# Kernel tuning notes

Measured on AMD Instinct MI355X. Metric: run time of the kernel, lower is better.

Reference implementation:

```python
import jax, jax.numpy as jnp
import numpy as np

B, L, T = 64, 128, 48
E, HE, H = 512, 1024, 1024


def setup_inputs() -> dict:
    key = jax.random.key(0)
    ks = jax.random.split(key, 20)
    s = 0.02
    inp = {
        'enc_hiddens': jax.random.normal(ks[0], (B, L, HE), jnp.float32),
        'enc_masks': jax.random.randint(ks[1], (B, L), 0, 2, jnp.int32),
        'h1_init': jax.random.normal(ks[2], (B, H), jnp.float32),
        'c1_init': jax.random.normal(ks[3], (B, H), jnp.float32),
        'h2_init': jax.random.normal(ks[4], (B, H), jnp.float32),
        'c2_init': jax.random.normal(ks[5], (B, H), jnp.float32),
        'captions': jax.random.normal(ks[6], (T, B, E), jnp.float32),
        # LSTMCell 1: input E -> hidden H
        'W_ih1': jax.random.normal(ks[7], (4 * H, E), jnp.float32) * s,
        'W_hh1': jax.random.normal(ks[8], (4 * H, H), jnp.float32) * s,
        'b_ih1': jnp.zeros((4 * H,), jnp.float32),
        'b_hh1': jnp.zeros((4 * H,), jnp.float32),
        # LSTMCell 2: input 2H -> hidden H
        'W_ih2': jax.random.normal(ks[9], (4 * H, 2 * H), jnp.float32) * s,
        'W_hh2': jax.random.normal(ks[10], (4 * H, H), jnp.float32) * s,
        'b_ih2': jnp.zeros((4 * H,), jnp.float32),
        'b_hh2': jnp.zeros((4 * H,), jnp.float32),
        # att_projection: He -> H
        'W_att': jax.random.normal(ks[11], (H, HE), jnp.float32) * s,
        'b_att': jnp.zeros((H,), jnp.float32),
        # combined_output_projection: He+H -> H
        'W_comb': jax.random.normal(ks[12], (H, HE + H), jnp.float32) * s,
        'b_comb': jnp.zeros((H,), jnp.float32),
    }
    return inp


def _lstm_cell(x, h, c, W_ih, W_hh, b_ih, b_hh):
    gates = x @ W_ih.T + b_ih + h @ W_hh.T + b_hh  # (B, 4H)
    i, f, g, o = jnp.split(gates, 4, axis=-1)
    i = jax.nn.sigmoid(i)
    f = jax.nn.sigmoid(f)
    g = jnp.tanh(g)
    o = jax.nn.sigmoid(o)
    c_new = f * c + i * g
    h_new = o * jnp.tanh(c_new)
    return h_new, c_new


def reference(enc_hiddens, enc_masks, h1_init, c1_init, h2_init, c2_init, captions,
              W_ih1, W_hh1, b_ih1, b_hh1, W_ih2, W_hh2, b_ih2, b_hh2,
              W_att, b_att, W_comb, b_comb):
    # Precompute attention projection of encoder hiddens: (B, L, H)
    enc_proj = jnp.einsum('blf,hf->blh', enc_hiddens, W_att) + b_att
    mask = enc_masks.astype(bool)  # True -> masked with -inf
    o0 = jnp.zeros((enc_hiddens.shape[0], W_hh1.shape[1]), enc_hiddens.dtype)

    def step(carry, elem):
        h1, c1, h2, c2, o_prev = carry
        h1, c1 = _lstm_cell(elem, h1, c1, W_ih1, W_hh1, b_ih1, b_hh1)
        bar = jnp.concatenate([h1, o_prev], axis=1)  # (B, 2H)
        h2, c2 = _lstm_cell(bar, h2, c2, W_ih2, W_hh2, b_ih2, b_hh2)
        e_t = jnp.einsum('bh,blh->bl', h2, enc_proj)
        e_t = jnp.where(mask, -jnp.inf, e_t)
        alpha = jax.nn.softmax(e_t, axis=1)
        a_t = jnp.einsum('bl,blf->bf', alpha, enc_hiddens)  # (B, He)
        U_t = jnp.concatenate([a_t, h2], axis=1)
        o_t = jnp.tanh(U_t @ W_comb.T + b_comb)  # dropout is identity in eval
        return (h1, c1, h2, c2, o_t), o_t

    _, outs = jax.lax.scan(step, (h1_init, c1_init, h2_init, c2_init, o0), captions)
    return outs  # (T, B, H)
```

## Files before the change

kernel.cpp:

```cpp
#include <hip/hip_runtime.h>

static constexpr int Bn = 64, Ln = 128, Tn = 48, En = 512, HEn = 1024, Hn = 1024, Gn = 4096;

typedef _Float16 h16;
typedef __attribute__((ext_vector_type(8))) _Float16 h16x8;
typedef __attribute__((ext_vector_type(2))) _Float16 h16x2;
typedef __attribute__((ext_vector_type(4))) float f32x4;

__device__ __forceinline__ float sigf(float x){ return 1.f / (1.f + expf(-x)); }

__device__ __forceinline__ h16x8 ldnt(const h16* p){
#if __has_builtin(__builtin_nontemporal_load)
  return __builtin_nontemporal_load(reinterpret_cast<const h16x8*>(p));
#else
  return *reinterpret_cast<const h16x8*>(p);
#endif
}

struct CvtJobs {
  const float* src[8];
  h16x2* dst[8];
  int n2[8];
};

__global__ void cvt_all(CvtJobs jobs){
  int stride = gridDim.x * blockDim.x;
  int gid = blockIdx.x * blockDim.x + threadIdx.x;
  #pragma unroll
  for (int s = 0; s < 8; s++){
    const float* src = jobs.src[s];
    h16x2* dst = jobs.dst[s];
    int n2 = jobs.n2[s];
    for (int i = gid; i < n2; i += stride){
      float2 v = reinterpret_cast<const float2*>(src)[i];
      h16x2 o; o.x = (h16)v.x; o.y = (h16)v.y;
      dst[i] = o;
    }
  }
}

__global__ void init_state(const float* __restrict__ h1i, const float* __restrict__ c1i,
                           const float* __restrict__ h2i, const float* __restrict__ c2i,
                           h16* __restrict__ h1a, float* __restrict__ c1,
                           h16* __restrict__ h2a, float* __restrict__ c2,
                           float* __restrict__ h2f, h16* __restrict__ oh){
  int i = blockIdx.x * blockDim.x + threadIdx.x;
  if (i < Bn * Hn){
    h1a[i] = (h16)h1i[i]; c1[i] = c1i[i];
    h2a[i] = (h16)h2i[i]; c2[i] = c2i[i];
    h2f[i] = h2i[i];
    oh[i] = (h16)0.f;
  }
}

__global__ __launch_bounds__(256, 2) void gemm_lds(
    const h16* __restrict__ A, int lda,
    const h16* __restrict__ Bw, int ldb,
    const float* __restrict__ bias0, const float* __restrict__ bias1,
    float* __restrict__ outF, h16* __restrict__ outH, int ldc, int K)
{
  __shared__ __align__(16) h16 sA[2][4096];
  __shared__ __align__(16) h16 sB[2][4096];
  int tid = threadIdx.x;
  int w = tid >> 6, lane = tid & 63;
  int la = lane & 15, q = lane >> 4;
  int wr = w >> 1, wc = w & 1;
  int m0 = blockIdx.x * 128, n0 = blockIdx.y * 128;

  int srow = tid >> 2, sq = tid & 3;
  const h16* gAa = A + (size_t)(m0 + srow) * lda + sq * 8;
  const h16* gAb = gAa + (size_t)64 * lda;
  const h16* gBa = Bw + (size_t)(n0 + srow) * ldb + sq * 8;
  const h16* gBb = gBa + (size_t)64 * ldb;
  int dO = sq * 1024 + srow * 8;

  f32x4 acc[4][4];
  #pragma unroll
  for (int i = 0; i < 4; i++)
    #pragma unroll
    for (int j = 0; j < 4; j++) acc[i][j] = (f32x4){0.f, 0.f, 0.f, 0.f};

  h16x8 rAa, rAb, rBa, rBb;
  auto GLOAD = [&](int kt){
    int k0 = kt * 32;
    rAa = *reinterpret_cast<const h16x8*>(gAa + k0);
    rAb = *reinterpret_cast<const h16x8*>(gAb + k0);
    rBa = *reinterpret_cast<const h16x8*>(gBa + k0);
    rBb = *reinterpret_cast<const h16x8*>(gBb + k0);
  };
  auto SWRITE = [&](int buf){
    *reinterpret_cast<h16x8*>(&sA[buf][dO])       = rAa;
    *reinterpret_cast<h16x8*>(&sA[buf][dO + 512]) = rAb;
    *reinterpret_cast<h16x8*>(&sB[buf][dO])       = rBa;
    *reinterpret_cast<h16x8*>(&sB[buf][dO + 512]) = rBb;
  };

  int NT = K / 32;
  GLOAD(0); SWRITE(0);
  GLOAD(1);
  __syncthreads();
  for (int t = 0; t < NT; t++){
    int buf = t & 1;
    h16x8 af[4], bf[4];
    #pragma unroll
    for (int mi = 0; mi < 4; mi++)
      af[mi] = *reinterpret_cast<const h16x8*>(&sA[buf][q * 1024 + (wr * 64 + mi * 16 + la) * 8]);
    #pragma unroll
    for (int ni = 0; ni < 4; ni++)
      bf[ni] = *reinterpret_cast<const h16x8*>(&sB[buf][q * 1024 + (wc * 64 + ni * 16 + la) * 8]);
    #pragma unroll
    for (int mi = 0; mi < 4; mi++)
      #pragma unroll
      for (int ni = 0; ni < 4; ni++)
        acc[mi][ni] = __builtin_amdgcn_mfma_f32_16x16x32_f16(af[mi], bf[ni], acc[mi][ni], 0, 0, 0);
    if (t + 1 < NT){
      __syncthreads();
      SWRITE((t + 1) & 1);
      if (t + 2 < NT) GLOAD(t + 2);
      __syncthreads();
    }
  }

  #pragma unroll
  for (int mi = 0; mi < 4; mi++){
    int mrow = m0 + wr * 64 + mi * 16 + q * 4;
    #pragma unroll
    for (int ni = 0; ni < 4; ni++){
      int n = n0 + wc * 64 + ni * 16 + la;
      float bs = (bias0 ? bias0[n] : 0.f) + (bias1 ? bias1[n] : 0.f);
      #pragma unroll
      for (int r = 0; r < 4; r++){
        float v = acc[mi][ni][r] + bs;
        size_t off = (size_t)(mrow + r) * ldc + n;
        if (outF) outF[off] = v;
        else      outH[off] = (h16)v;
      }
    }
  }
}

struct PBuf { h16x8 a0, a1, a2, a3, b; };

__device__ __forceinline__ void pld(PBuf& p, const h16* __restrict__ Ap,
                                    const h16* __restrict__ Bp, int k){
  p.a0 = *reinterpret_cast<const h16x8*>(Ap + k);
  p.a1 = *reinterpret_cast<const h16x8*>(Ap + 16 * Hn + k);
  p.a2 = *reinterpret_cast<const h16x8*>(Ap + 32 * Hn + k);
  p.a3 = *reinterpret_cast<const h16x8*>(Ap + 48 * Hn + k);
  p.b  = *reinterpret_cast<const h16x8*>(Bp + k);
}
__device__ __forceinline__ void pmm(const PBuf& p, f32x4* acc){
  acc[0] = __builtin_amdgcn_mfma_f32_16x16x32_f16(p.a0, p.b, acc[0], 0, 0, 0);
  acc[1] = __builtin_amdgcn_mfma_f32_16x16x32_f16(p.a1, p.b, acc[1], 0, 0, 0);
  acc[2] = __builtin_amdgcn_mfma_f32_16x16x32_f16(p.a2, p.b, acc[2], 0, 0, 0);
  acc[3] = __builtin_amdgcn_mfma_f32_16x16x32_f16(p.a3, p.b, acc[3], 0, 0, 0);
}

template<int NS>
__device__ __forceinline__ void gseg_pf(const h16* __restrict__ Ap,
                                        const h16* __restrict__ Bp, f32x4* acc){
  PBuf p0, p1, p2, p3;
  pld(p0, Ap, Bp, 0);
  pld(p1, Ap, Bp, 32);
  pld(p2, Ap, Bp, 64);
  pld(p3, Ap, Bp, 96);
  #pragma unroll 1
  for (int s = 0; s + 4 < NS; s += 4){
    pmm(p0, acc); pld(p0, Ap, Bp, (s + 4) * 32);
    pmm(p1, acc); pld(p1, Ap, Bp, (s + 5) * 32);
    pmm(p2, acc); pld(p2, Ap, Bp, (s + 6) * 32);
    pmm(p3, acc); pld(p3, Ap, Bp, (s + 7) * 32);
  }
  pmm(p0, acc); pmm(p1, acc); pmm(p2, acc); pmm(p3, acc);
}

struct PBuf2 { h16x8 a0, a1, b; };

__device__ __forceinline__ void pld2(PBuf2& p, const h16* __restrict__ Ap,
                                     const h16* __restrict__ Bp, int k){
  p.a0 = *reinterpret_cast<const h16x8*>(Ap + k);
  p.a1 = *reinterpret_cast<const h16x8*>(Ap + 16 * Hn + k);
  p.b  = ldnt(Bp + k);
}
__device__ __forceinline__ void pmm2(const PBuf2& p, f32x4* acc){
  acc[0] = __builtin_amdgcn_mfma_f32_16x16x32_f16(p.a0, p.b, acc[0], 0, 0, 0);
  acc[1] = __builtin_amdgcn_mfma_f32_16x16x32_f16(p.a1, p.b, acc[1], 0, 0, 0);
}

template<int NS>
__device__ __forceinline__ void gseg2_pf(const h16* __restrict__ Ap,
                                         const h16* __restrict__ Bp, f32x4* acc){
  PBuf2 p0, p1, p2, p3;
  pld2(p0, Ap, Bp, 0);
  pld2(p1, Ap, Bp, 32);
  pld2(p2, Ap, Bp, 64);
  pld2(p3, Ap, Bp, 96);
  #pragma unroll 1
  for (int s = 0; s + 4 < NS; s += 4){
    pmm2(p0, acc); pld2(p0, Ap, Bp, (s + 4) * 32);
    pmm2(p1, acc); pld2(p1, Ap, Bp, (s + 5) * 32);
    pmm2(p2, acc); pld2(p2, Ap, Bp, (s + 6) * 32);
    pmm2(p3, acc); pld2(p3, Ap, Bp, (s + 7) * 32);
  }
  pmm2(p0, acc); pmm2(p1, acc); pmm2(p2, acc); pmm2(p3, acc);
}

__global__ __launch_bounds__(512, 1) void kA(
    const h16* __restrict__ h1cur, const h16* __restrict__ h2prev, const h16* __restrict__ oh,
    h16* __restrict__ h1next, h16* __restrict__ h2cur, float* __restrict__ h2f,
    float* __restrict__ c1, float* __restrict__ c2,
    const h16* __restrict__ wih2, const h16* __restrict__ whh2, const h16* __restrict__ whh1,
    const float* __restrict__ bih2, const float* __restrict__ bhh2,
    const float* __restrict__ pre1_t, int mode)
{
  __shared__ float sg[4][2][32][17];
  int bid = blockIdx.x, tid = threadIdx.x;
  int wv = tid >> 6, lane = tid & 63;
  int g = wv & 3, kh = wv >> 2;
  int la = lane & 15, q = lane >> 4;
  bool is2 = (mode == 1) && (bid < 128);
  int unit = is2 ? bid : (mode == 1 ? bid - 128 : bid);
  int jb = unit & 63, mh = unit >> 6;
  int j0 = jb * 16;
  int r0 = mh * 32;
  bool active = is2 || (pre1_t != nullptr);

  if (active){
    f32x4 acc[2];
    acc[0] = (f32x4){0.f, 0.f, 0.f, 0.f};
    acc[1] = (f32x4){0.f, 0.f, 0.f, 0.f};
    int n0 = g * 1024 + j0;
    size_t aoff = (size_t)(r0 + la) * Hn + q * 8;
    if (is2){
      if (kh == 0){
        gseg2_pf<32>(h1cur + aoff, wih2 + (size_t)(n0 + la) * 2048 + q * 8,        acc);
        gseg2_pf<16>(oh    + aoff, wih2 + (size_t)(n0 + la) * 2048 + 1024 + q * 8, acc);
      } else {
        gseg2_pf<16>(oh     + aoff + 512, wih2 + (size_t)(n0 + la) * 2048 + 1536 + q * 8, acc);
        gseg2_pf<32>(h2prev + aoff,       whh2 + (size_t)(n0 + la) * 1024 + q * 8,        acc);
      }
    } else {
      if (kh == 0)
        gseg2_pf<16>(h1cur + aoff,       whh1 + (size_t)(n0 + la) * 1024 + q * 8,       acc);
      else
        gseg2_pf<16>(h1cur + aoff + 512, whh1 + (size_t)(n0 + la) * 1024 + 512 + q * 8, acc);
    }
    #pragma unroll
    for (int mi = 0; mi < 2; mi++)
      #pragma unroll
      for (int r = 0; r < 4; r++)
        sg[g][kh][mi * 16 + q * 4 + r][la] = acc[mi][r];
  }
  __syncthreads();
  if (active && tid < 512){
    int e = tid;
    int rl = e >> 4, col = e & 15, j = j0 + col;
    int row = r0 + rl;
    float gi = sg[0][0][rl][col] + sg[0][1][rl][col];
    float gf = sg[1][0][rl][col] + sg[1][1][rl][col];
    float gg = sg[2][0][rl][col] + sg[2][1][rl][col];
    float go = sg[3][0][rl][col] + sg[3][1][rl][col];
    if (is2){
      gi += bih2[j] + bhh2[j];
      gf += bih2[j + 1024] + bhh2[j + 1024];
      gg += bih2[j + 2048] + bhh2[j + 2048];
      go += bih2[j + 3072] + bhh2[j + 3072];
      float c_ = sigf(gf) * c2[row * Hn + j] + sigf(gi) * tanhf(gg);
      c2[row * Hn + j] = c_;
      float h_ = sigf(go) * tanhf(c_);
      h2cur[row * Hn + j] = (h16)h_;
      h2f[row * Hn + j] = h_;
    } else {
      const float* p = pre1_t + (size_t)row * Gn;
      gi += p[j]; gf += p[j + 1024]; gg += p[j + 2048]; go += p[j + 3072];
      float c_ = sigf(gf) * c1[row * Hn + j] + sigf(gi) * tanhf(gg);
      c1[row * Hn + j] = c_;
      h1next[row * Hn + j] = (h16)(sigf(go) * tanhf(c_));
    }
  }
}

__global__ __launch_bounds__(256, 2) void kB(
    const float* __restrict__ h2f, const h16* __restrict__ eph, const int* __restrict__ msk,
    float* __restrict__ ebuf,
    const h16* __restrict__ h2cur, const h16* __restrict__ wcomb, const float* __restrict__ bcomb,
    float* __restrict__ hwb)
{
  int bid = blockIdx.x, tid = threadIdx.x;
  int w = tid >> 6, lane = tid & 63;
  if (bid >= 16){
    int n = bid - 16;
    int b = n & 63;
    int l = (n >> 6) * 4 + w;
    const f32x4* h2r = reinterpret_cast<const f32x4*>(h2f + (size_t)b * Hn + lane * 16);
    f32x4 hv0 = h2r[0], hv1 = h2r[1], hv2 = h2r[2], hv3 = h2r[3];
    const h16x8* er = reinterpret_cast<const h16x8*>(eph + ((size_t)b * Ln + l) * Hn + lane * 16);
    h16x8 e0 = er[0], e1 = er[1];
    float acc = 0.f;
    #pragma unroll
    for (int i = 0; i < 4; i++) acc += hv0[i] * (float)e0[i];
    #pragma unroll
    for (int i = 0; i < 4; i++) acc += hv1[i] * (float)e0[4 + i];
    #pragma unroll
    for (int i = 0; i < 4; i++) acc += hv2[i] * (float)e1[i];
    #pragma unroll
    for (int i = 0; i < 4; i++) acc += hv3[i] * (float)e1[4 + i];
    for (int off = 32; off; off >>= 1) acc += __shfl_xor(acc, off);
    if (lane == 0) ebuf[b * Ln + l] = msk[b * Ln + l] ? -1e30f : acc;
  } else {
    int hb = bid;
    int la = lane & 15, q = lane >> 4;
    int n0 = hb * 64 + w * 16;
    f32x4 acc[4];
    #pragma unroll
    for (int mi = 0; mi < 4; mi++) acc[mi] = (f32x4){0.f, 0.f, 0.f, 0.f};
    gseg_pf<32>(h2cur + la * Hn + q * 8,
                wcomb + (size_t)(n0 + la) * (HEn + Hn) + HEn + q * 8, acc);
    float bs = bcomb[n0 + la];
    #pragma unroll
    for (int mi = 0; mi < 4; mi++)
      #pragma unroll
      for (int r = 0; r < 4; r++)
        hwb[(size_t)(mi * 16 + q * 4 + r) * Hn + n0 + la] = acc[mi][r] + bs;
  }
}

__global__ __launch_bounds__(256, 2) void kC(
    int t, const float* __restrict__ ebuf,
    const h16* __restrict__ ecbh, const float* __restrict__ hwb,
    float* __restrict__ out, h16* __restrict__ oh)
{
  __shared__ float sb[Ln];
  __shared__ float rmax[4], rsum[4];
  __shared__ float sp[128][2];
  int bid = blockIdx.x;
  int b = bid & 63;
  int jq = (bid >> 6) * 256;
  int tid = threadIdx.x;
  int wv = tid >> 6;
  float e = ebuf[b * Ln + (tid & 127)];
  float m = e;
  #pragma unroll
  for (int off = 32; off; off >>= 1) m = fmaxf(m, __shfl_xor(m, off));
  if ((tid & 63) == 0) rmax[wv] = m;
  __syncthreads();
  m = fmaxf(fmaxf(rmax[0], rmax[1]), fmaxf(rmax[2], rmax[3]));
  float ex = expf(e - m);
  if (tid < 128) sb[tid] = ex;
  float s = ex;
  #pragma unroll
  for (int off = 32; off; off >>= 1) s += __shfl_xor(s, off);
  if ((tid & 63) == 0) rsum[wv] = s;
  __syncthreads();
  float rinv = 1.f / (rsum[0] + rsum[1]);

  int col = tid & 127, lh = tid >> 7;
  int j0 = jq + col * 2;
  const h16* base = ecbh + (size_t)b * Ln * Hn + j0;
  float a0 = 0.f, a1 = 0.f, c0 = 0.f, c1 = 0.f;
  int lb = lh * 64;
  #pragma unroll 8
  for (int i = 0; i < 64; i += 2){
    int l = lb + i;
    float al0 = sb[l], al1 = sb[l + 1];
    h16x2 p0 = *reinterpret_cast<const h16x2*>(base + (size_t)l * Hn);
    h16x2 p1 = *reinterpret_cast<const h16x2*>(base + (size_t)(l + 1) * Hn);
    a0 += al0 * (float)p0.x; a1 += al0 * (float)p0.y;
    c0 += al1 * (float)p1.x; c1 += al1 * (float)p1.y;
  }
  float t0 = a0 + c0, t1 = a1 + c1;
  if (lh == 1){ sp[col][0] = t0; sp[col][1] = t1; }
  __syncthreads();
  if (lh == 0){
    float g0 = (t0 + sp[col][0]) * rinv;
    float g1 = (t1 + sp[col][1]) * rinv;
    float2 hw2 = *reinterpret_cast<const float2*>(hwb + b * Hn + j0);
    float o0 = tanhf(g0 + hw2.x);
    float o1 = tanhf(g1 + hw2.y);
    *reinterpret_cast<float2*>(out + ((size_t)t * Bn + b) * Hn + j0) = make_float2(o0, o1);
    h16x2 opk; opk.x = (h16)o0; opk.y = (h16)o1;
    *reinterpret_cast<h16x2*>(oh + (size_t)b * Hn + j0) = opk;
  }
}

extern "C" void kernel_launch(void* const* d_in, const int* in_sizes, int n_in,
                              void* d_out, int out_size, void* d_ws, size_t ws_size,
                              hipStream_t stream)
{
  const float* enc   = (const float*)d_in[0];
  const int*   msk   = (const int*)  d_in[1];
  const float* h1i   = (const float*)d_in[2];
  const float* c1i   = (const float*)d_in[3];
  const float* h2i   = (const float*)d_in[4];
  const float* c2i   = (const float*)d_in[5];
  const float* caps  = (const float*)d_in[6];
  const float* Wih1  = (const float*)d_in[7];
  const float* Whh1  = (const float*)d_in[8];
  const float* bih1  = (const float*)d_in[9];
  const float* bhh1  = (const float*)d_in[10];
  const float* Wih2  = (const float*)d_in[11];
  const float* Whh2  = (const float*)d_in[12];
  const float* bih2  = (const float*)d_in[13];
  const float* bhh2  = (const float*)d_in[14];
  const float* Watt  = (const float*)d_in[15];
  const float* batt  = (const float*)d_in[16];
  const float* Wcomb = (const float*)d_in[17];
  const float* bcomb = (const float*)d_in[18];
  float* out = (float*)d_out;

  char* p = (char*)d_ws;
  auto take = [&](size_t bytes){ char* r = p; p += (bytes + 255) & ~(size_t)255; return r; };
  float* pre1   = (float*)take((size_t)Tn * Bn * Gn * 4);
  h16*   ench   = (h16*)take((size_t)Bn * Ln * HEn * 2);
  h16*   eph    = (h16*)take((size_t)Bn * Ln * Hn * 2);
  h16*   ecbh   = (h16*)take((size_t)Bn * Ln * Hn * 2);
  h16*   caph   = (h16*)take((size_t)Tn * Bn * En * 2);
  h16*   wih1h  = (h16*)take((size_t)Gn * En * 2);
  h16*   whh1h  = (h16*)take((size_t)Gn * Hn * 2);
  h16*   wih2h  = (h16*)take((size_t)Gn * 2 * Hn * 2);
  h16*   whh2h  = (h16*)take((size_t)Gn * Hn * 2);
  h16*   watth  = (h16*)take((size_t)Hn * HEn * 2);
  h16*   wcombh = (h16*)take((size_t)Hn * (HEn + Hn) * 2);
  h16*   h1b0   = (h16*)take((size_t)Bn * Hn * 2);
  h16*   h1b1   = (h16*)take((size_t)Bn * Hn * 2);
  h16*   h2b0   = (h16*)take((size_t)Bn * Hn * 2);
  h16*   h2b1   = (h16*)take((size_t)Bn * Hn * 2);
  h16*   oh     = (h16*)take((size_t)Bn * Hn * 2);
  float* c1     = (float*)take((size_t)Bn * Hn * 4);
  float* c2     = (float*)take((size_t)Bn * Hn * 4);
  float* h2f    = (float*)take((size_t)Bn * Hn * 4);
  float* ebuf   = (float*)take((size_t)Bn * Ln * 4);
  float* hwb    = (float*)take((size_t)Bn * Hn * 4);
  (void)ws_size; (void)n_in; (void)in_sizes; (void)out_size;

  CvtJobs jobs;
  jobs.src[0] = enc;   jobs.dst[0] = (h16x2*)ench;   jobs.n2[0] = Bn * Ln * HEn / 2;
  jobs.src[1] = caps;  jobs.dst[1] = (h16x2*)caph;   jobs.n2[1] = Tn * Bn * En / 2;
  jobs.src[2] = Wih1;  jobs.dst[2] = (h16x2*)wih1h;  jobs.n2[2] = Gn * En / 2;
  jobs.src[3] = Whh1;  jobs.dst[3] = (h16x2*)whh1h;  jobs.n2[3] = Gn * Hn / 2;
  jobs.src[4] = Wih2;  jobs.dst[4] = (h16x2*)wih2h;  jobs.n2[4] = Gn * 2 * Hn / 2;
  jobs.src[5] = Whh2;  jobs.dst[5] = (h16x2*)whh2h;  jobs.n2[5] = Gn * Hn / 2;
  jobs.src[6] = Watt;  jobs.dst[6] = (h16x2*)watth;  jobs.n2[6] = Hn * HEn / 2;
  jobs.src[7] = Wcomb; jobs.dst[7] = (h16x2*)wcombh; jobs.n2[7] = Hn * (HEn + Hn) / 2;
  cvt_all<<<2048, 256, 0, stream>>>(jobs);

  init_state<<<(Bn * Hn) / 256, 256, 0, stream>>>(h1i, c1i, h2i, c2i,
                                                  h1b0, c1, h2b0, c2, h2f, oh);

  gemm_lds<<<dim3((Tn * Bn) / 128, Gn / 128), 256, 0, stream>>>(
      caph, En, wih1h, En, bih1, bhh1, pre1, nullptr, Gn, En);
  gemm_lds<<<dim3((Bn * Ln) / 128, Hn / 128), 256, 0, stream>>>(
      ench, HEn, watth, HEn, batt, nullptr, nullptr, eph, Hn, HEn);
  gemm_lds<<<dim3((Bn * Ln) / 128, Hn / 128), 256, 0, stream>>>(
      ench, HEn, wcombh, HEn + Hn, nullptr, nullptr, nullptr, ecbh, Hn, HEn);

  kA<<<128, 512, 0, stream>>>(h1b0, h2b0, oh, h1b1, h2b1, h2f, c1, c2,
                              wih2h, whh2h, whh1h, bih2, bhh2, pre1, 0);

  h16* h1buf[2] = { h1b0, h1b1 };
  h16* h2buf[2] = { h2b0, h2b1 };
  for (int t = 0; t < Tn; t++){
    h16* h1cur  = h1buf[(t + 1) & 1];
    h16* h1next = h1buf[t & 1];
    h16* h2prev = h2buf[t & 1];
    h16* h2cur  = h2buf[(t + 1) & 1];
    const float* pre1_t = (t + 1 < Tn) ? (pre1 + (size_t)(t + 1) * Bn * Gn) : nullptr;
    kA<<<256, 512, 0, stream>>>(h1cur, h2prev, oh, h1next, h2cur, h2f, c1, c2,
                                wih2h, whh2h, whh1h, bih2, bhh2, pre1_t, 1);
    kB<<<2064, 256, 0, stream>>>(h2f, eph, msk, ebuf, h2cur, wcombh, bcomb, hwb);
    kC<<<256, 256, 0, stream>>>(t, ebuf, ecbh, hwb, out, oh);
  }
}
```

Before: 3.260 ms.

## Stage LSTM gate GEMM operands through double-buffered LDS tiles in kA

Replaces the per-wave direct-from-global register prefetch pipeline (with nontemporal weight loads) by a block-cooperative scheme. Each 128-column K chunk of the activations and weights is loaded once into double-buffered shared memory, and the waves read their MFMA fragments from LDS. The aim is coalesced, non-redundant global loads and a simpler pipeline. In exchange it adds two block-wide barriers per K step and only one stage of lookahead, which may expose memory latency in this latency-bound recurrent kernel.

```diff
diff --git a/kernel.cpp b/kernel.cpp
--- a/kernel.cpp
+++ b/kernel.cpp
@@ -8,14 +8,6 @@
 typedef __attribute__((ext_vector_type(4))) float f32x4;
 
 __device__ __forceinline__ float sigf(float x){ return 1.f / (1.f + expf(-x)); }
-
-__device__ __forceinline__ h16x8 ldnt(const h16* p){
-#if __has_builtin(__builtin_nontemporal_load)
-  return __builtin_nontemporal_load(reinterpret_cast<const h16x8*>(p));
-#else
-  return *reinterpret_cast<const h16x8*>(p);
-#endif
-}
 
 struct CvtJobs {
   const float* src[8];
@@ -174,37 +166,6 @@
   pmm(p0, acc); pmm(p1, acc); pmm(p2, acc); pmm(p3, acc);
 }
 
-struct PBuf2 { h16x8 a0, a1, b; };
-
-__device__ __forceinline__ void pld2(PBuf2& p, const h16* __restrict__ Ap,
-                                     const h16* __restrict__ Bp, int k){
-  p.a0 = *reinterpret_cast<const h16x8*>(Ap + k);
-  p.a1 = *reinterpret_cast<const h16x8*>(Ap + 16 * Hn + k);
-  p.b  = ldnt(Bp + k);
-}
-__device__ __forceinline__ void pmm2(const PBuf2& p, f32x4* acc){
-  acc[0] = __builtin_amdgcn_mfma_f32_16x16x32_f16(p.a0, p.b, acc[0], 0, 0, 0);
-  acc[1] = __builtin_amdgcn_mfma_f32_16x16x32_f16(p.a1, p.b, acc[1], 0, 0, 0);
-}
-
-template<int NS>
-__device__ __forceinline__ void gseg2_pf(const h16* __restrict__ Ap,
-                                         const h16* __restrict__ Bp, f32x4* acc){
-  PBuf2 p0, p1, p2, p3;
-  pld2(p0, Ap, Bp, 0);
-  pld2(p1, Ap, Bp, 32);
-  pld2(p2, Ap, Bp, 64);
-  pld2(p3, Ap, Bp, 96);
-  #pragma unroll 1
-  for (int s = 0; s + 4 < NS; s += 4){
-    pmm2(p0, acc); pld2(p0, Ap, Bp, (s + 4) * 32);
-    pmm2(p1, acc); pld2(p1, Ap, Bp, (s + 5) * 32);
-    pmm2(p2, acc); pld2(p2, Ap, Bp, (s + 6) * 32);
-    pmm2(p3, acc); pld2(p3, Ap, Bp, (s + 7) * 32);
-  }
-  pmm2(p0, acc); pmm2(p1, acc); pmm2(p2, acc); pmm2(p3, acc);
-}
-
 __global__ __launch_bounds__(512, 1) void kA(
     const h16* __restrict__ h1cur, const h16* __restrict__ h2prev, const h16* __restrict__ oh,
     h16* __restrict__ h1next, h16* __restrict__ h2cur, float* __restrict__ h2f,
@@ -213,6 +174,8 @@
     const float* __restrict__ bih2, const float* __restrict__ bhh2,
     const float* __restrict__ pre1_t, int mode)
 {
+  __shared__ __align__(16) h16 sA[2][4096];
+  __shared__ __align__(16) h16 sB[2][8192];
   __shared__ float sg[4][2][32][17];
   int bid = blockIdx.x, tid = threadIdx.x;
   int wv = tid >> 6, lane = tid & 63;
@@ -226,30 +189,65 @@
   bool active = is2 || (pre1_t != nullptr);
 
   if (active){
-    f32x4 acc[2];
-    acc[0] = (f32x4){0.f, 0.f, 0.f, 0.f};
-    acc[1] = (f32x4){0.f, 0.f, 0.f, 0.f};
-    int n0 = g * 1024 + j0;
-    size_t aoff = (size_t)(r0 + la) * Hn + q * 8;
-    if (is2){
-      if (kh == 0){
-        gseg2_pf<32>(h1cur + aoff, wih2 + (size_t)(n0 + la) * 2048 + q * 8,        acc);
-        gseg2_pf<16>(oh    + aoff, wih2 + (size_t)(n0 + la) * 2048 + 1024 + q * 8, acc);
-      } else {
-        gseg2_pf<16>(oh     + aoff + 512, wih2 + (size_t)(n0 + la) * 2048 + 1536 + q * 8, acc);
-        gseg2_pf<32>(h2prev + aoff,       whh2 + (size_t)(n0 + la) * 1024 + q * 8,        acc);
+    f32x4 acc0 = (f32x4){0.f, 0.f, 0.f, 0.f};
+    f32x4 acc1 = (f32x4){0.f, 0.f, 0.f, 0.f};
+    int NT = is2 ? 24 : 8;
+
+    int sa_cc = tid & 15, sa_row = tid >> 4;
+    int sb_cc0 = tid & 15, sb_grl0 = tid >> 4;
+    int t1 = tid + 512;
+    int sb_cc1 = t1 & 15, sb_grl1 = t1 >> 4;
+
+    h16x8 rA, rB0, rB1;
+    auto GLOAD = [&](int st){
+      int fc = st * 128;
+      const h16* pa;
+      if (!is2)            pa = h1cur + fc;
+      else if (fc < 1024)  pa = h1cur + fc;
+      else if (fc < 2048)  pa = oh + (fc - 1024);
+      else                 pa = h2prev + (fc - 2048);
+      rA = *reinterpret_cast<const h16x8*>(pa + (size_t)(r0 + sa_row) * Hn + sa_cc * 8);
+      const h16* pb; int bstr;
+      if (!is2){ pb = whh1 + fc; bstr = 1024; }
+      else if (fc < 2048){ pb = wih2 + fc; bstr = 2048; }
+      else { pb = whh2 + (fc - 2048); bstr = 1024; }
+      rB0 = *reinterpret_cast<const h16x8*>(
+          pb + (size_t)((sb_grl0 >> 4) * 1024 + j0 + (sb_grl0 & 15)) * bstr + sb_cc0 * 8);
+      rB1 = *reinterpret_cast<const h16x8*>(
+          pb + (size_t)((sb_grl1 >> 4) * 1024 + j0 + (sb_grl1 & 15)) * bstr + sb_cc1 * 8);
+    };
+    auto SWRITE = [&](int buf){
+      *reinterpret_cast<h16x8*>(&sA[buf][(sa_cc * 32 + sa_row) * 8])  = rA;
+      *reinterpret_cast<h16x8*>(&sB[buf][(sb_cc0 * 64 + sb_grl0) * 8]) = rB0;
+      *reinterpret_cast<h16x8*>(&sB[buf][(sb_cc1 * 64 + sb_grl1) * 8]) = rB1;
+    };
+
+    GLOAD(0); SWRITE(0);
+    GLOAD(1);
+    __syncthreads();
+    for (int st = 0; st < NT; st++){
+      int buf = st & 1;
+      #pragma unroll
+      for (int uu = 0; uu < 2; uu++){
+        int cc = (kh * 2 + uu) * 4 + q;
+        h16x8 a0 = *reinterpret_cast<const h16x8*>(&sA[buf][(cc * 32 + la) * 8]);
+        h16x8 a1 = *reinterpret_cast<const h16x8*>(&sA[buf][(cc * 32 + 16 + la) * 8]);
+        h16x8 bf = *reinterpret_cast<const h16x8*>(&sB[buf][(cc * 64 + g * 16 + la) * 8]);
+        acc0 = __builtin_amdgcn_mfma_f32_16x16x32_f16(a0, bf, acc0, 0, 0, 0);
+        acc1 = __builtin_amdgcn_mfma_f32_16x16x32_f16(a1, bf, acc1, 0, 0, 0);
       }
-    } else {
-      if (kh == 0)
-        gseg2_pf<16>(h1cur + aoff,       whh1 + (size_t)(n0 + la) * 1024 + q * 8,       acc);
-      else
-        gseg2_pf<16>(h1cur + aoff + 512, whh1 + (size_t)(n0 + la) * 1024 + 512 + q * 8, acc);
-    }
-    #pragma unroll
-    for (int mi = 0; mi < 2; mi++)
-      #pragma unroll
-      for (int r = 0; r < 4; r++)
-        sg[g][kh][mi * 16 + q * 4 + r][la] = acc[mi][r];
+      if (st + 1 < NT){
+        __syncthreads();
+        SWRITE((st + 1) & 1);
+        if (st + 2 < NT) GLOAD(st + 2);
+        __syncthreads();
+      }
+    }
+    #pragma unroll
+    for (int r = 0; r < 4; r++){
+      sg[g][kh][q * 4 + r][la]      = acc0[r];
+      sg[g][kh][16 + q * 4 + r][la] = acc1[r];
+    }
   }
   __syncthreads();
   if (active && tid < 512){
```

Result: faster. 2.658 ms (-18.5%).
